# Optimization experiments

Hardware: AMD Instinct MI355X
Metric: run time of the kernel (lower is better)

## Reference

```python
import jax, jax.numpy as jnp
import numpy as np

B, R, D, H, C = 256, 100, 6168, 128, 100  # batch, replicas, in_dim, hidden, classes


def setup_inputs() -> dict:
    key = jax.random.key(0)
    k1, k2, k3, k4, k5, k6 = jax.random.split(key, 6)
    # binary input features (texas dataset is binary; original casts to bool)
    x = jax.random.randint(k1, (B, D), 0, 2).astype(jnp.int32)
    # Bernoulli(0.5) flip mask, one per replica per feature
    noise = jax.random.randint(k2, (B, R, D), 0, 2).astype(jnp.int32)
    s1 = 1.0 / np.sqrt(D)
    W1 = jax.random.uniform(k3, (D, H), minval=-s1, maxval=s1, dtype=jnp.float32)
    b1 = jax.random.uniform(k4, (H,), minval=-s1, maxval=s1, dtype=jnp.float32)
    s2 = 1.0 / np.sqrt(H)
    W2 = jax.random.uniform(k5, (H, C), minval=-s2, maxval=s2, dtype=jnp.float32)
    b2 = jax.random.uniform(k6, (C,), minval=-s2, maxval=s2, dtype=jnp.float32)
    return {"x": x, "noise": noise, "W1": W1, "b1": b1, "W2": W2, "b2": b2}


def reference(x, noise, W1, b1, W2, b2):
    # np.invert(x, where=noise) on booleans == flip bit where noise==1
    xb = x[:, None, :]                                   # [B,1,D]
    x_noisy = jnp.where(noise == 1, 1 - xb, xb).astype(W1.dtype)  # [B,R,D]
    h = jnp.tanh(jnp.einsum('brd,dh->brh', x_noisy, W1) + b1)      # [B,R,H]
    logits = jnp.einsum('brh,hc->brc', h, W2) + b2                 # [B,R,C]
    return logits.mean(axis=1)                                     # [B,C]
```

## Files before the change

### kernel.cpp

```cpp
#include <hip/hip_runtime.h>
#include <hip/hip_bf16.h>

#define NB 256
#define NR 100
#define ND 6168
#define DP 6176
#define NH 128
#define NC 100
#define CP 112
#define KSTEP 32
#define NSTEP (DP / KSTEP)
#define MT 128

typedef __attribute__((ext_vector_type(8))) __bf16 bf16x8;
typedef __attribute__((ext_vector_type(4))) float f32x4;
typedef __attribute__((ext_vector_type(4))) int i32x4;
typedef __attribute__((ext_vector_type(4))) unsigned int u32x4;

__global__ void prep_w1t(const float* __restrict__ W1, __hip_bfloat16* __restrict__ W1T) {
  __shared__ float tile[KSTEP][NH + 1];
  const int d0 = blockIdx.x * KSTEP;
  const int t = threadIdx.x;
#pragma unroll
  for (int p = 0; p < (KSTEP * NH) / 256; ++p) {
    int idx = p * 256 + t;
    int dd = idx >> 7;
    int h  = idx & 127;
    int d  = d0 + dd;
    tile[dd][h] = (d < ND) ? W1[d * NH + h] : 0.f;
  }
  __syncthreads();
#pragma unroll
  for (int p = 0; p < (KSTEP * NH) / 256; ++p) {
    int idx = p * 256 + t;
    int h  = idx >> 5;
    int dd = idx & 31;
    W1T[h * DP + d0 + dd] = __float2bfloat16(tile[dd][h]);
  }
}

__global__ void prep_w2t(const float* __restrict__ W2, __hip_bfloat16* __restrict__ W2T) {
  int t = blockIdx.x * 256 + threadIdx.x;
  if (t < CP * NH) {
    int c = t >> 7;
    int h = t & 127;
    float v = (c < NC) ? W2[h * NC + c] : 0.f;
    W2T[t] = __float2bfloat16(v);
  }
}

__launch_bounds__(256, 1)
__global__ void fused_main(const int* __restrict__ x,
                           const int* __restrict__ noise,
                           const __hip_bfloat16* __restrict__ W1T,
                           const float* __restrict__ b1,
                           const __hip_bfloat16* __restrict__ W2T,
                           const float* __restrict__ b2,
                           float* __restrict__ out) {
  __shared__ __align__(16) char lds[41984];
  unsigned int* xbits = (unsigned int*)lds;

  const int tid  = threadIdx.x;
  const int lane = tid & 63;
  const int w    = tid >> 6;
  const int b    = blockIdx.x;

  const int r    = tid >> 1;
  const int koff = (tid & 1) * 16;
  const bool rvalid = (r < NR);
  const long nbase = (long)b * NR * ND + (long)r * ND;

  char* const A0 = lds + 1024;
  char* const A1 = A0 + 10240;
  char* const B0 = A1 + 10240;
  char* const B1 = B0 + 10240;

  f32x4 acc[8][2] = {};

  auto LOAD_A = [&](int s, i32x4* areg) {
    const int k0 = s * KSTEP;
#pragma unroll
    for (int j = 0; j < 4; ++j) {
      int c = k0 + koff + j * 4;
      i32x4 v = {0, 0, 0, 0};
      if (rvalid && c < ND) v = *(const i32x4*)(noise + nbase + c);
      areg[j] = v;
    }
  };
  auto LOAD_B = [&](int s, i32x4* breg) {
    const char* src = (const char*)W1T + ((long)r * DP + s * KSTEP) * 2 + (tid & 1) * 32;
    breg[0] = *(const i32x4*)(src);
    breg[1] = *(const i32x4*)(src + 16);
  };
  auto STORE_A = [&](int s, const i32x4* areg, char* Al) {
    unsigned int xw = rvalid ? (xbits[s] >> koff) : 0u;
    unsigned int pk[8];
#pragma unroll
    for (int j = 0; j < 4; ++j) {
#pragma unroll
      for (int e = 0; e < 2; ++e) {
        unsigned v0 = ((unsigned)areg[j][e * 2]     ^ (xw >> (j * 4 + e * 2)))     & 1u;
        unsigned v1 = ((unsigned)areg[j][e * 2 + 1] ^ (xw >> (j * 4 + e * 2 + 1))) & 1u;
        pk[j * 2 + e] = (v0 ? 0x3F80u : 0u) | (v1 ? 0x3F800000u : 0u);
      }
    }
    u32x4* dst = (u32x4*)(Al + r * 80 + koff * 2);
    u32x4 t0 = {pk[0], pk[1], pk[2], pk[3]};
    u32x4 t1 = {pk[4], pk[5], pk[6], pk[7]};
    dst[0] = t0;
    dst[1] = t1;
  };
  auto STORE_B = [&](const i32x4* breg, char* Bl) {
    i32x4* dst = (i32x4*)(Bl + r * 80 + (tid & 1) * 32);
    dst[0] = breg[0];
    dst[1] = breg[1];
  };
  auto COMPUTE = [&](const char* Al, const char* Bl) {
    const int lq = lane >> 4;
    const int lm = lane & 15;
    bf16x8 bf0 = *(const bf16x8*)(Bl + (w * 32 + lm) * 80 + lq * 16);
    bf16x8 bf1 = *(const bf16x8*)(Bl + (w * 32 + 16 + lm) * 80 + lq * 16);
#pragma unroll
    for (int mf = 0; mf < 8; ++mf) {
      bf16x8 af = *(const bf16x8*)(Al + (mf * 16 + lm) * 80 + lq * 16);
      acc[mf][0] = __builtin_amdgcn_mfma_f32_16x16x32_bf16(af, bf0, acc[mf][0], 0, 0, 0);
      acc[mf][1] = __builtin_amdgcn_mfma_f32_16x16x32_bf16(af, bf1, acc[mf][1], 0, 0, 0);
    }
  };

  i32x4 ra0[4], ra1[4], rb0[2], rb1[2];

  LOAD_A(0, ra0); LOAD_B(0, rb0);
  LOAD_A(1, ra1); LOAD_B(1, rb1);
  {
    unsigned long long* xq = (unsigned long long*)lds;
    const int* xb = x + b * ND;
    for (int q = w; q < DP / 64 + 1; q += 4) {
      int d = q * 64 + lane;
      int v = (d < ND) ? xb[d] : 0;
      unsigned long long m = __ballot(v != 0);
      if (lane == 0) xq[q] = m;
    }
  }
  __syncthreads();
  STORE_A(0, ra0, A0); STORE_B(rb0, B0);
  __syncthreads();

  for (int s = 0; s < NSTEP; s += 2) {
    if (s + 2 < NSTEP) { LOAD_A(s + 2, ra0); LOAD_B(s + 2, rb0); }
    COMPUTE(A0, B0);
    if (s + 1 < NSTEP) { STORE_A(s + 1, ra1, A1); STORE_B(rb1, B1); }
    __syncthreads();
    if (s + 3 < NSTEP) { LOAD_A(s + 3, ra1); LOAD_B(s + 3, rb1); }
    if (s + 1 < NSTEP) COMPUTE(A1, B1);
    if (s + 2 < NSTEP) { STORE_A(s + 2, ra0, A0); STORE_B(rb0, B0); }
    __syncthreads();
  }

  __hip_bfloat16* h_tile = (__hip_bfloat16*)lds;
  float* partial = (float*)(lds + 34816);
  const int lq = lane >> 4;
  const int lm = lane & 15;

#pragma unroll
  for (int nf = 0; nf < 2; ++nf) {
    int hcol = w * 32 + nf * 16 + lm;
    float bb = b1[hcol];
#pragma unroll
    for (int mf = 0; mf < 8; ++mf) {
#pragma unroll
      for (int rg = 0; rg < 4; ++rg) {
        int m = mf * 16 + lq * 4 + rg;
        float hv = tanhf(acc[mf][nf][rg] + bb);
        h_tile[m * 136 + hcol] = __float2bfloat16(hv);
      }
    }
  }
  __syncthreads();

  f32x4 acc2[2][7] = {};
#pragma unroll
  for (int ks = 0; ks < 4; ++ks) {
    bf16x8 a2_0 = *(const bf16x8*)((const unsigned short*)h_tile + (w * 32 + lm) * 136 + ks * 32 + lq * 8);
    bf16x8 a2_1 = *(const bf16x8*)((const unsigned short*)h_tile + (w * 32 + 16 + lm) * 136 + ks * 32 + lq * 8);
#pragma unroll
    for (int nf = 0; nf < 7; ++nf) {
      bf16x8 b2f = *(const bf16x8*)((const unsigned short*)W2T + (nf * 16 + lm) * NH + ks * 32 + lq * 8);
      acc2[0][nf] = __builtin_amdgcn_mfma_f32_16x16x32_bf16(a2_0, b2f, acc2[0][nf], 0, 0, 0);
      acc2[1][nf] = __builtin_amdgcn_mfma_f32_16x16x32_bf16(a2_1, b2f, acc2[1][nf], 0, 0, 0);
    }
  }

#pragma unroll
  for (int mf2 = 0; mf2 < 2; ++mf2) {
    int mbase = w * 32 + mf2 * 16 + lq * 4;
#pragma unroll
    for (int nf = 0; nf < 7; ++nf) {
      float ssum = 0.f;
#pragma unroll
      for (int rg = 0; rg < 4; ++rg) {
        int m = mbase + rg;
        ssum += (m < NR) ? acc2[mf2][nf][rg] : 0.f;
      }
      ssum += __shfl_xor(ssum, 16, 64);
      ssum += __shfl_xor(ssum, 32, 64);
      if (lq == 0) partial[(w * 2 + mf2) * 112 + nf * 16 + lm] = ssum;
    }
  }
  __syncthreads();

  if (tid < NC) {
    float fsum = 0.f;
#pragma unroll
    for (int p = 0; p < 8; ++p) fsum += partial[p * 112 + tid];
    out[b * NC + tid] = fsum * (1.f / NR) + b2[tid];
  }
}

extern "C" void kernel_launch(void* const* d_in, const int* in_sizes, int n_in,
                              void* d_out, int out_size, void* d_ws, size_t ws_size,
                              hipStream_t stream) {
  (void)in_sizes; (void)n_in; (void)out_size; (void)ws_size;
  const int* x     = (const int*)d_in[0];
  const int* noise = (const int*)d_in[1];
  const float* W1  = (const float*)d_in[2];
  const float* b1  = (const float*)d_in[3];
  const float* W2  = (const float*)d_in[4];
  const float* b2  = (const float*)d_in[5];
  float* out = (float*)d_out;

  __hip_bfloat16* W1T = (__hip_bfloat16*)d_ws;
  __hip_bfloat16* W2T = (__hip_bfloat16*)((char*)d_ws + (size_t)NH * DP * 2);

  prep_w1t<<<DP / KSTEP, 256, 0, stream>>>(W1, W1T);
  prep_w2t<<<(CP * NH + 255) / 256, 256, 0, stream>>>(W2, W2T);
  fused_main<<<NB, 256, 0, stream>>>(x, noise, W1T, b1, W2T, b2, out);
}
```

Before: 244.4 us.

## Use 512-thread blocks with 4-stage LDS pipeline and cheaper bit-flip packing

Doubles the block to 8 waves arranged as a 2x4 wave grid over the 128x128 first GEMM tile, so each wave holds half the accumulators. The main loop now cycles through four LDS stages instead of two, with global loads issued further ahead to hide memory latency on the dominant noise stream. The x bits are pre-expanded into paired 16-bit lanes so the XOR-and-convert to bf16 is a single multiply per two elements. The cost is larger LDS use (about 94KB) and more barriers per block.

```diff
diff --git a/kernel.cpp b/kernel.cpp
--- a/kernel.cpp
+++ b/kernel.cpp
@@ -10,7 +10,6 @@
 #define CP 112
 #define KSTEP 32
 #define NSTEP (DP / KSTEP)
-#define MT 128
 
 typedef __attribute__((ext_vector_type(8))) __bf16 bf16x8;
 typedef __attribute__((ext_vector_type(4))) float f32x4;
@@ -49,7 +48,7 @@
   }
 }
 
-__launch_bounds__(256, 1)
+__launch_bounds__(512, 1)
 __global__ void fused_main(const int* __restrict__ x,
                            const int* __restrict__ noise,
                            const __hip_bfloat16* __restrict__ W1T,
@@ -57,155 +56,156 @@
                            const __hip_bfloat16* __restrict__ W2T,
                            const float* __restrict__ b2,
                            float* __restrict__ out) {
-  __shared__ __align__(16) char lds[41984];
-  unsigned int* xbits = (unsigned int*)lds;
+  __shared__ __align__(16) char lds[94272];
+  unsigned int* xpair = (unsigned int*)lds;
+  char* const bufbase = lds + 12352;
+  char* const BF0 = bufbase;
+  char* const BF1 = bufbase + 20480;
+  char* const BF2 = bufbase + 40960;
+  char* const BF3 = bufbase + 61440;
 
   const int tid  = threadIdx.x;
   const int lane = tid & 63;
   const int w    = tid >> 6;
+  const int wm   = w >> 2;
+  const int wn   = w & 3;
+  const int lq   = lane >> 4;
+  const int lm   = lane & 15;
   const int b    = blockIdx.x;
 
-  const int r    = tid >> 1;
-  const int koff = (tid & 1) * 16;
+  const int r  = tid >> 2;
+  const int kc = tid & 3;
   const bool rvalid = (r < NR);
-  const long nbase = (long)b * NR * ND + (long)r * ND;
-
-  char* const A0 = lds + 1024;
-  char* const A1 = A0 + 10240;
-  char* const B0 = A1 + 10240;
-  char* const B1 = B0 + 10240;
-
-  f32x4 acc[8][2] = {};
-
-  auto LOAD_A = [&](int s, i32x4* areg) {
-    const int k0 = s * KSTEP;
+
+  const int*  nbase = noise + (long)b * NR * ND + (long)r * ND + kc * 8;
+  const char* bsrc  = (const char*)W1T + (long)r * DP * 2 + kc * 16;
+
+  f32x4 acc[4][2] = {};
+
+  auto ISSUE = [&](int s, i32x4* ra, i32x4* rb) {
+    const int k0 = s * KSTEP + kc * 8;
+    i32x4 z = {0, 0, 0, 0};
+    ra[0] = (rvalid && k0 + 4 <= ND) ? *(const i32x4*)(nbase + (long)s * KSTEP)     : z;
+    ra[1] = (rvalid && k0 + 8 <= ND) ? *(const i32x4*)(nbase + (long)s * KSTEP + 4) : z;
+    rb[0] = *(const i32x4*)(bsrc + (long)s * 64);
+  };
+
+  auto STORE = [&](int s, const i32x4* ra, const i32x4* rb, char* buf) {
+    u32x4 xp = *(const u32x4*)(xpair + s * 16 + kc * 4);
+    unsigned int pk[4];
 #pragma unroll
     for (int j = 0; j < 4; ++j) {
-      int c = k0 + koff + j * 4;
-      i32x4 v = {0, 0, 0, 0};
-      if (rvalid && c < ND) v = *(const i32x4*)(noise + nbase + c);
-      areg[j] = v;
-    }
+      unsigned n0 = (unsigned)ra[j >> 1][(j & 1) * 2];
+      unsigned n1 = (unsigned)ra[j >> 1][(j & 1) * 2 + 1];
+      pk[j] = ((n0 | (n1 << 16)) ^ xp[j]) * 0x3F80u;
+    }
+    u32x4 t = {pk[0], pk[1], pk[2], pk[3]};
+    *(u32x4*)(buf + r * 80 + kc * 16) = t;
+    *(i32x4*)(buf + 10240 + r * 80 + kc * 16) = rb[0];
   };
-  auto LOAD_B = [&](int s, i32x4* breg) {
-    const char* src = (const char*)W1T + ((long)r * DP + s * KSTEP) * 2 + (tid & 1) * 32;
-    breg[0] = *(const i32x4*)(src);
-    breg[1] = *(const i32x4*)(src + 16);
-  };
-  auto STORE_A = [&](int s, const i32x4* areg, char* Al) {
-    unsigned int xw = rvalid ? (xbits[s] >> koff) : 0u;
-    unsigned int pk[8];
-#pragma unroll
-    for (int j = 0; j < 4; ++j) {
-#pragma unroll
-      for (int e = 0; e < 2; ++e) {
-        unsigned v0 = ((unsigned)areg[j][e * 2]     ^ (xw >> (j * 4 + e * 2)))     & 1u;
-        unsigned v1 = ((unsigned)areg[j][e * 2 + 1] ^ (xw >> (j * 4 + e * 2 + 1))) & 1u;
-        pk[j * 2 + e] = (v0 ? 0x3F80u : 0u) | (v1 ? 0x3F800000u : 0u);
-      }
-    }
-    u32x4* dst = (u32x4*)(Al + r * 80 + koff * 2);
-    u32x4 t0 = {pk[0], pk[1], pk[2], pk[3]};
-    u32x4 t1 = {pk[4], pk[5], pk[6], pk[7]};
-    dst[0] = t0;
-    dst[1] = t1;
-  };
-  auto STORE_B = [&](const i32x4* breg, char* Bl) {
-    i32x4* dst = (i32x4*)(Bl + r * 80 + (tid & 1) * 32);
-    dst[0] = breg[0];
-    dst[1] = breg[1];
-  };
-  auto COMPUTE = [&](const char* Al, const char* Bl) {
-    const int lq = lane >> 4;
-    const int lm = lane & 15;
-    bf16x8 bf0 = *(const bf16x8*)(Bl + (w * 32 + lm) * 80 + lq * 16);
-    bf16x8 bf1 = *(const bf16x8*)(Bl + (w * 32 + 16 + lm) * 80 + lq * 16);
-#pragma unroll
-    for (int mf = 0; mf < 8; ++mf) {
-      bf16x8 af = *(const bf16x8*)(Al + (mf * 16 + lm) * 80 + lq * 16);
+
+  auto COMPUTE = [&](const char* buf) {
+    const char* A  = buf;
+    const char* Bb = buf + 10240;
+    bf16x8 bf0 = *(const bf16x8*)(Bb + (wn * 32 + lm) * 80 + lq * 16);
+    bf16x8 bf1 = *(const bf16x8*)(Bb + (wn * 32 + 16 + lm) * 80 + lq * 16);
+#pragma unroll
+    for (int mf = 0; mf < 4; ++mf) {
+      bf16x8 af = *(const bf16x8*)(A + (wm * 64 + mf * 16 + lm) * 80 + lq * 16);
       acc[mf][0] = __builtin_amdgcn_mfma_f32_16x16x32_bf16(af, bf0, acc[mf][0], 0, 0, 0);
       acc[mf][1] = __builtin_amdgcn_mfma_f32_16x16x32_bf16(af, bf1, acc[mf][1], 0, 0, 0);
     }
   };
 
-  i32x4 ra0[4], ra1[4], rb0[2], rb1[2];
-
-  LOAD_A(0, ra0); LOAD_B(0, rb0);
-  LOAD_A(1, ra1); LOAD_B(1, rb1);
+  i32x4 raA[2], rbA[1], raB[2], rbB[1];
+
+  ISSUE(0, raA, rbA);
+  ISSUE(1, raB, rbB);
   {
-    unsigned long long* xq = (unsigned long long*)lds;
     const int* xb = x + b * ND;
-    for (int q = w; q < DP / 64 + 1; q += 4) {
-      int d = q * 64 + lane;
-      int v = (d < ND) ? xb[d] : 0;
-      unsigned long long m = __ballot(v != 0);
-      if (lane == 0) xq[q] = m;
-    }
-  }
-  __syncthreads();
-  STORE_A(0, ra0, A0); STORE_B(rb0, B0);
-  __syncthreads();
-
-  for (int s = 0; s < NSTEP; s += 2) {
-    if (s + 2 < NSTEP) { LOAD_A(s + 2, ra0); LOAD_B(s + 2, rb0); }
-    COMPUTE(A0, B0);
-    if (s + 1 < NSTEP) { STORE_A(s + 1, ra1, A1); STORE_B(rb1, B1); }
-    __syncthreads();
-    if (s + 3 < NSTEP) { LOAD_A(s + 3, ra1); LOAD_B(s + 3, rb1); }
-    if (s + 1 < NSTEP) COMPUTE(A1, B1);
-    if (s + 2 < NSTEP) { STORE_A(s + 2, ra0, A0); STORE_B(rb0, B0); }
-    __syncthreads();
-  }
-
-  __hip_bfloat16* h_tile = (__hip_bfloat16*)lds;
-  float* partial = (float*)(lds + 34816);
-  const int lq = lane >> 4;
-  const int lm = lane & 15;
+    for (int i = tid; i < DP / 2; i += 512) {
+      unsigned p = 0;
+      if (2 * i < ND) {
+        int2 v = *(const int2*)(xb + 2 * i);
+        p = ((unsigned)v.x & 1u) | (((unsigned)v.y & 1u) << 16);
+      }
+      xpair[i] = p;
+    }
+  }
+  __syncthreads();
+  STORE(0, raA, rbA, BF0);
+  ISSUE(2, raA, rbA);
+  STORE(1, raB, rbB, BF1);
+  __syncthreads();
+
+  for (int s = 0; s < NSTEP; s += 4) {
+    {
+      COMPUTE(BF0);
+      if (s + 3 < NSTEP) ISSUE(s + 3, raB, rbB);
+      if (s + 2 < NSTEP) STORE(s + 2, raA, rbA, BF2);
+      __syncthreads();
+    }
+    if (s + 1 < NSTEP) {
+      COMPUTE(BF1);
+      if (s + 4 < NSTEP) ISSUE(s + 4, raA, rbA);
+      if (s + 3 < NSTEP) STORE(s + 3, raB, rbB, BF3);
+      __syncthreads();
+    }
+    if (s + 2 < NSTEP) {
+      COMPUTE(BF2);
+      if (s + 5 < NSTEP) ISSUE(s + 5, raB, rbB);
+      if (s + 4 < NSTEP) STORE(s + 4, raA, rbA, BF0);
+      __syncthreads();
+    }
+    if (s + 3 < NSTEP) {
+      COMPUTE(BF3);
+      if (s + 6 < NSTEP) ISSUE(s + 6, raA, rbA);
+      if (s + 5 < NSTEP) STORE(s + 5, raB, rbB, BF1);
+      __syncthreads();
+    }
+  }
+  __syncthreads();
+
+  __hip_bfloat16* h_tile = (__hip_bfloat16*)(lds + 12352);
+  float* partial = (float*)(lds + 12352 + 34816);
 
 #pragma unroll
   for (int nf = 0; nf < 2; ++nf) {
-    int hcol = w * 32 + nf * 16 + lm;
+    int hcol = wn * 32 + nf * 16 + lm;
     float bb = b1[hcol];
 #pragma unroll
-    for (int mf = 0; mf < 8; ++mf) {
+    for (int mf = 0; mf < 4; ++mf) {
 #pragma unroll
       for (int rg = 0; rg < 4; ++rg) {
-        int m = mf * 16 + lq * 4 + rg;
-        float hv = tanhf(acc[mf][nf][rg] + bb);
-        h_tile[m * 136 + hcol] = __float2bfloat16(hv);
+        int m = wm * 64 + mf * 16 + lq * 4 + rg;
+        h_tile[m * 136 + hcol] = __float2bfloat16(tanhf(acc[mf][nf][rg] + bb));
       }
     }
   }
   __syncthreads();
 
-  f32x4 acc2[2][7] = {};
+  f32x4 acc2[7] = {};
 #pragma unroll
   for (int ks = 0; ks < 4; ++ks) {
-    bf16x8 a2_0 = *(const bf16x8*)((const unsigned short*)h_tile + (w * 32 + lm) * 136 + ks * 32 + lq * 8);
-    bf16x8 a2_1 = *(const bf16x8*)((const unsigned short*)h_tile + (w * 32 + 16 + lm) * 136 + ks * 32 + lq * 8);
+    bf16x8 a2 = *(const bf16x8*)((const unsigned short*)h_tile + (w * 16 + lm) * 136 + ks * 32 + lq * 8);
 #pragma unroll
     for (int nf = 0; nf < 7; ++nf) {
       bf16x8 b2f = *(const bf16x8*)((const unsigned short*)W2T + (nf * 16 + lm) * NH + ks * 32 + lq * 8);
-      acc2[0][nf] = __builtin_amdgcn_mfma_f32_16x16x32_bf16(a2_0, b2f, acc2[0][nf], 0, 0, 0);
-      acc2[1][nf] = __builtin_amdgcn_mfma_f32_16x16x32_bf16(a2_1, b2f, acc2[1][nf], 0, 0, 0);
-    }
-  }
-
-#pragma unroll
-  for (int mf2 = 0; mf2 < 2; ++mf2) {
-    int mbase = w * 32 + mf2 * 16 + lq * 4;
-#pragma unroll
-    for (int nf = 0; nf < 7; ++nf) {
-      float ssum = 0.f;
-#pragma unroll
-      for (int rg = 0; rg < 4; ++rg) {
-        int m = mbase + rg;
-        ssum += (m < NR) ? acc2[mf2][nf][rg] : 0.f;
-      }
-      ssum += __shfl_xor(ssum, 16, 64);
-      ssum += __shfl_xor(ssum, 32, 64);
-      if (lq == 0) partial[(w * 2 + mf2) * 112 + nf * 16 + lm] = ssum;
-    }
+      acc2[nf] = __builtin_amdgcn_mfma_f32_16x16x32_bf16(a2, b2f, acc2[nf], 0, 0, 0);
+    }
+  }
+
+#pragma unroll
+  for (int nf = 0; nf < 7; ++nf) {
+    float ssum = 0.f;
+#pragma unroll
+    for (int rg = 0; rg < 4; ++rg) {
+      int m = w * 16 + lq * 4 + rg;
+      ssum += (m < NR) ? acc2[nf][rg] : 0.f;
+    }
+    ssum += __shfl_xor(ssum, 16, 64);
+    ssum += __shfl_xor(ssum, 32, 64);
+    if (lq == 0) partial[w * 112 + nf * 16 + lm] = ssum;
   }
   __syncthreads();
 
@@ -234,5 +234,5 @@
 
   prep_w1t<<<DP / KSTEP, 256, 0, stream>>>(W1, W1T);
   prep_w2t<<<(CP * NH + 255) / 256, 256, 0, stream>>>(W2, W2T);
-  fused_main<<<NB, 256, 0, stream>>>(x, noise, W1T, b1, W2T, b2, out);
-}
+  fused_main<<<NB, 512, 0, stream>>>(x, noise, W1T, b1, W2T, b2, out);
+}
```

Measured after the change: 271.0 us. 10.9% more time.
